# Performance work log

Measured on AMD Instinct MI355X. Metric: run time of the kernel, lower is better.

## Reference

```python
import jax, jax.numpy as jnp
import numpy as np

POLY_DEGREE = 3
LOW, MID, HIGH = 3, 6, 9
K = LOW + MID + HIGH  # 18 total harmonics
NUM_POINTS = 128 ** 3
BATCH = 4


def _band_sum(t, a, b, omega):
    """sum_k a_k*cos(w_k t) + b_k*sin(w_k t) without materializing [B,N,K].
    t: [B,N]; a,b: [N,k]; omega: [k]. Scans over the small harmonic axis."""
    def step(acc, xs):
        a_k, b_k, w = xs  # a_k,b_k: [N], w: scalar
        ph = w * t  # [B,N]
        return acc + a_k[None, :] * jnp.cos(ph) + b_k[None, :] * jnp.sin(ph), None
    acc0 = jnp.zeros_like(t)
    acc, _ = jax.lax.scan(step, acc0, (a.T, b.T, omega))
    return acc


def setup_inputs() -> dict:
    key = jax.random.key(0)
    k1, k2, k3, k4 = jax.random.split(key, 4)
    input_t = jax.random.uniform(k1, (BATCH,), dtype=jnp.float32)  # times in [0,1)
    poly_coeffs = jax.random.normal(k2, (NUM_POINTS, POLY_DEGREE + 1), dtype=jnp.float32) * 0.1
    fourier_a = jax.random.normal(k3, (NUM_POINTS, K), dtype=jnp.float32) * 0.1
    fourier_b = jax.random.normal(k4, (NUM_POINTS, K), dtype=jnp.float32) * 0.1
    return {
        "input_t": input_t,
        "poly_coeffs": poly_coeffs,
        "fourier_a": fourier_a,
        "fourier_b": fourier_b,
        "model_stage": 3,
    }


def reference(input_t, poly_coeffs, fourier_a, fourier_b, model_stage):
    B = input_t.shape[0]
    N = poly_coeffs.shape[0]
    t = jnp.broadcast_to(input_t[:, None], (B, N))  # [B, N]
    curr_stage = min(model_stage, 3) if model_stage >= 0 else 3
    omega = 2.0 * jnp.pi * jnp.arange(1, K + 1, dtype=jnp.float32)

    y_poly = jnp.zeros((B, N), dtype=jnp.float32)
    if POLY_DEGREE > 0 and curr_stage >= 0:
        for i in range(POLY_DEGREE + 1):
            y_poly = y_poly + poly_coeffs[:, i][None, :] * t ** i

    y_fourier = jnp.zeros((B, N), dtype=jnp.float32)
    bands = [(0, LOW, 1), (LOW, LOW + MID, 2), (LOW + MID, K, 3)]
    for s, e, req_stage in bands:
        if e > s and curr_stage >= req_stage:
            y_fourier = y_fourier + _band_sum(
                t, fourier_a[:, s:e], fourier_b[:, s:e], omega[s:e]
            )
    return y_poly, y_fourier
```

## Files before the change

### kernel.cpp

```cpp
#include <hip/hip_runtime.h>

#define KH 18
#define NPTS (128*128*128)
#define BB 4
#define BLK 256
#define ROW_FLOATS (BLK * KH)

__global__ __launch_bounds__(256, 4) void dddm_kernel(
    const float* __restrict__ input_t,
    const float* __restrict__ poly,
    const float* __restrict__ fa,
    const float* __restrict__ fb,
    const int*   __restrict__ stage_p,
    float* __restrict__ out)
{
    __shared__ float s[2 * ROW_FLOATS];
    __shared__ float ct[BB][KH];
    __shared__ float st[BB][KH];
    __shared__ float tp[BB][4];

    const int tid = threadIdx.x;
    const int n0  = blockIdx.x * BLK;

    if (tid < BB * KH) {
        const int b = tid / KH, k = tid % KH;
        const float t = input_t[b];
        const float ph = 6.283185307179586f * (float)(k + 1) * t;
        float sn, cs;
        sincosf(ph, &sn, &cs);
        ct[b][k] = cs;
        st[b][k] = sn;
    } else if (tid < BB * KH + BB) {
        const int b = tid - BB * KH;
        const float t = input_t[b];
        tp[b][0] = 1.0f;
        tp[b][1] = t;
        tp[b][2] = t * t;
        tp[b][3] = t * t * t;
    }

    const float4* fa4 = reinterpret_cast<const float4*>(fa + (size_t)n0 * KH);
    const float4* fb4 = reinterpret_cast<const float4*>(fb + (size_t)n0 * KH);
    float4* s4 = reinterpret_cast<float4*>(s);

    float4 v[9];
#pragma unroll
    for (int j = 0; j < 9; ++j) {
        const int idx = j * BLK + tid;
        v[j] = (idx < ROW_FLOATS / 4) ? fa4[idx] : fb4[idx - ROW_FLOATS / 4];
    }
#pragma unroll
    for (int j = 0; j < 9; ++j) {
        const int idx = j * BLK + tid;
        s4[idx] = v[j];
    }

    const int ms = *stage_p;
    const int cs = (ms >= 0) ? (ms < 3 ? ms : 3) : 3;
    const int kmax = (cs >= 3) ? 18 : (cs == 2 ? 9 : (cs == 1 ? 3 : 0));

    __syncthreads();

    const int n = n0 + tid;

    const float4 c4 = reinterpret_cast<const float4*>(poly)[n];
    float yp[BB];
#pragma unroll
    for (int b = 0; b < BB; ++b)
        yp[b] = c4.x * tp[b][0] + c4.y * tp[b][1] + c4.z * tp[b][2] + c4.w * tp[b][3];

    float av[KH], bv[KH];
    {
        const float2* ar = reinterpret_cast<const float2*>(s + tid * KH);
        const float2* br = reinterpret_cast<const float2*>(s + ROW_FLOATS + tid * KH);
#pragma unroll
        for (int j = 0; j < 9; ++j) {
            const float2 a2 = ar[j];
            const float2 b2 = br[j];
            av[2 * j] = a2.x; av[2 * j + 1] = a2.y;
            bv[2 * j] = b2.x; bv[2 * j + 1] = b2.y;
        }
    }

    float yf[BB] = {0.f, 0.f, 0.f, 0.f};
    if (kmax == KH) {
#pragma unroll
        for (int k = 0; k < KH; ++k) {
            const float ak = av[k], bk = bv[k];
#pragma unroll
            for (int b = 0; b < BB; ++b)
                yf[b] += ak * ct[b][k] + bk * st[b][k];
        }
    } else if (kmax > 0) {
        for (int k = 0; k < kmax; ++k) {
            const float ak = av[k], bk = bv[k];
#pragma unroll
            for (int b = 0; b < BB; ++b)
                yf[b] += ak * ct[b][k] + bk * st[b][k];
        }
    }

#pragma unroll
    for (int b = 0; b < BB; ++b) {
        out[(size_t)b * NPTS + n]        = yp[b];
        out[(size_t)(BB + b) * NPTS + n] = yf[b];
    }
}

extern "C" void kernel_launch(void* const* d_in, const int* in_sizes, int n_in,
                              void* d_out, int out_size, void* d_ws, size_t ws_size,
                              hipStream_t stream) {
    const float* input_t = (const float*)d_in[0];
    const float* poly    = (const float*)d_in[1];
    const float* fa      = (const float*)d_in[2];
    const float* fb      = (const float*)d_in[3];
    const int*   stage   = (const int*)d_in[4];
    float* out = (float*)d_out;

    dddm_kernel<<<NPTS / BLK, BLK, 0, stream>>>(input_t, poly, fa, fb, stage, out);
}
```

Measured before the change: 352.1 us.

## Drop shared-memory staging; load Fourier rows directly and use Chebyshev recurrence

Removes the cooperative LDS staging of the fa/fb rows and the block barrier. Each thread now reads its own 72-byte rows with float2 loads straight from global memory. The per-block sincos table is replaced by a per-thread Chebyshev recurrence (cos/sin of k*w from the k=1 value), and the polynomial uses Horner form. Launch bounds are raised to allow more waves per CU. Direct strided per-thread loads are less coalesced, which relies on caches to merge them, and the recurrence may slightly change numerical accuracy.

```diff
diff --git a/kernel.cpp b/kernel.cpp
--- a/kernel.cpp
+++ b/kernel.cpp
@@ -4,9 +4,8 @@
 #define NPTS (128*128*128)
 #define BB 4
 #define BLK 256
-#define ROW_FLOATS (BLK * KH)
 
-__global__ __launch_bounds__(256, 4) void dddm_kernel(
+__global__ __launch_bounds__(BLK, 8) void dddm_kernel(
     const float* __restrict__ input_t,
     const float* __restrict__ poly,
     const float* __restrict__ fa,
@@ -14,89 +13,82 @@
     const int*   __restrict__ stage_p,
     float* __restrict__ out)
 {
-    __shared__ float s[2 * ROW_FLOATS];
-    __shared__ float ct[BB][KH];
-    __shared__ float st[BB][KH];
-    __shared__ float tp[BB][4];
+    const int tid = threadIdx.x;
+    const int n   = blockIdx.x * BLK + tid;
 
-    const int tid = threadIdx.x;
-    const int n0  = blockIdx.x * BLK;
-
-    if (tid < BB * KH) {
-        const int b = tid / KH, k = tid % KH;
+    float tb[BB], c1[BB], s1[BB], d[BB];
+#pragma unroll
+    for (int b = 0; b < BB; ++b) {
         const float t = input_t[b];
-        const float ph = 6.283185307179586f * (float)(k + 1) * t;
+        tb[b] = t;
         float sn, cs;
-        sincosf(ph, &sn, &cs);
-        ct[b][k] = cs;
-        st[b][k] = sn;
-    } else if (tid < BB * KH + BB) {
-        const int b = tid - BB * KH;
-        const float t = input_t[b];
-        tp[b][0] = 1.0f;
-        tp[b][1] = t;
-        tp[b][2] = t * t;
-        tp[b][3] = t * t * t;
-    }
-
-    const float4* fa4 = reinterpret_cast<const float4*>(fa + (size_t)n0 * KH);
-    const float4* fb4 = reinterpret_cast<const float4*>(fb + (size_t)n0 * KH);
-    float4* s4 = reinterpret_cast<float4*>(s);
-
-    float4 v[9];
-#pragma unroll
-    for (int j = 0; j < 9; ++j) {
-        const int idx = j * BLK + tid;
-        v[j] = (idx < ROW_FLOATS / 4) ? fa4[idx] : fb4[idx - ROW_FLOATS / 4];
-    }
-#pragma unroll
-    for (int j = 0; j < 9; ++j) {
-        const int idx = j * BLK + tid;
-        s4[idx] = v[j];
+        sincosf(6.283185307179586f * t, &sn, &cs);
+        c1[b] = cs; s1[b] = sn; d[b] = 2.0f * cs;
     }
 
     const int ms = *stage_p;
-    const int cs = (ms >= 0) ? (ms < 3 ? ms : 3) : 3;
-    const int kmax = (cs >= 3) ? 18 : (cs == 2 ? 9 : (cs == 1 ? 3 : 0));
-
-    __syncthreads();
-
-    const int n = n0 + tid;
+    const int cs_ = (ms >= 0) ? (ms < 3 ? ms : 3) : 3;
+    const int kmax = (cs_ >= 3) ? 18 : (cs_ == 2 ? 9 : (cs_ == 1 ? 3 : 0));
 
     const float4 c4 = reinterpret_cast<const float4*>(poly)[n];
-    float yp[BB];
+    float yp[BB], yf[BB];
 #pragma unroll
-    for (int b = 0; b < BB; ++b)
-        yp[b] = c4.x * tp[b][0] + c4.y * tp[b][1] + c4.z * tp[b][2] + c4.w * tp[b][3];
+    for (int b = 0; b < BB; ++b) {
+        const float t = tb[b];
+        yp[b] = ((c4.w * t + c4.z) * t + c4.y) * t + c4.x;
+        yf[b] = 0.0f;
+    }
 
-    float av[KH], bv[KH];
-    {
-        const float2* ar = reinterpret_cast<const float2*>(s + tid * KH);
-        const float2* br = reinterpret_cast<const float2*>(s + ROW_FLOATS + tid * KH);
+    const float2* ar = reinterpret_cast<const float2*>(fa + (size_t)n * KH);
+    const float2* br = reinterpret_cast<const float2*>(fb + (size_t)n * KH);
+
+    if (kmax == KH) {
+        float cc[BB], ss[BB], cp[BB], sp[BB];
+#pragma unroll
+        for (int b = 0; b < BB; ++b) {
+            cc[b] = c1[b]; ss[b] = s1[b];
+            cp[b] = 1.0f;  sp[b] = 0.0f;
+        }
 #pragma unroll
         for (int j = 0; j < 9; ++j) {
             const float2 a2 = ar[j];
             const float2 b2 = br[j];
-            av[2 * j] = a2.x; av[2 * j + 1] = a2.y;
-            bv[2 * j] = b2.x; bv[2 * j + 1] = b2.y;
-        }
-    }
-
-    float yf[BB] = {0.f, 0.f, 0.f, 0.f};
-    if (kmax == KH) {
 #pragma unroll
-        for (int k = 0; k < KH; ++k) {
-            const float ak = av[k], bk = bv[k];
+            for (int u = 0; u < 2; ++u) {
+                const float ak = u ? a2.y : a2.x;
+                const float bk = u ? b2.y : b2.x;
 #pragma unroll
-            for (int b = 0; b < BB; ++b)
-                yf[b] += ak * ct[b][k] + bk * st[b][k];
+                for (int b = 0; b < BB; ++b) {
+                    yf[b] += ak * cc[b];
+                    yf[b] += bk * ss[b];
+                    const float cn = __builtin_fmaf(d[b], cc[b], -cp[b]);
+                    const float s2 = __builtin_fmaf(d[b], ss[b], -sp[b]);
+                    cp[b] = cc[b]; sp[b] = ss[b];
+                    cc[b] = cn;    ss[b] = s2;
+                }
+            }
         }
     } else if (kmax > 0) {
+        const float* arow = fa + (size_t)n * KH;
+        const float* brow = fb + (size_t)n * KH;
+        float cc[BB], ss[BB], cp[BB], sp[BB];
+#pragma unroll
+        for (int b = 0; b < BB; ++b) {
+            cc[b] = c1[b]; ss[b] = s1[b];
+            cp[b] = 1.0f;  sp[b] = 0.0f;
+        }
         for (int k = 0; k < kmax; ++k) {
-            const float ak = av[k], bk = bv[k];
+            const float ak = arow[k];
+            const float bk = brow[k];
 #pragma unroll
-            for (int b = 0; b < BB; ++b)
-                yf[b] += ak * ct[b][k] + bk * st[b][k];
+            for (int b = 0; b < BB; ++b) {
+                yf[b] += ak * cc[b];
+                yf[b] += bk * ss[b];
+                const float cn = __builtin_fmaf(d[b], cc[b], -cp[b]);
+                const float s2 = __builtin_fmaf(d[b], ss[b], -sp[b]);
+                cp[b] = cc[b]; sp[b] = ss[b];
+                cc[b] = cn;    ss[b] = s2;
+            }
         }
     }
 
```

After: 374.3 us. 1.06x slower.
